# Kernel optimization log

Hardware: AMD Instinct MI355X
Metric: run time of the kernel (lower is better)

Reference implementation:

```python
import jax, jax.numpy as jnp
import numpy as np
import math

DIM = 1024
NUM_HEADS = 16
HEAD_DIM = DIM // NUM_HEADS
ROPE_BASE = 10000.0
LN_EPS = 1e-5


def _rope_tables(seq_len):
    inv_freq = 1.0 / (ROPE_BASE ** (jnp.arange(0, HEAD_DIM, 2, dtype=jnp.float32) / HEAD_DIM))
    t = jnp.arange(seq_len, dtype=jnp.float32)
    freqs = t[:, None] * inv_freq[None, :]            # (T, D/2)
    emb = jnp.concatenate([freqs, freqs], axis=-1)    # (T, D)
    return jnp.cos(emb), jnp.sin(emb)


def _rotate_half(x):
    x1 = x[..., ::2]
    x2 = x[..., 1::2]
    return jnp.stack((-x2, x1), axis=-1).reshape(x.shape)


def _heads(y):
    B, T, _ = y.shape
    return y.reshape(B, T, NUM_HEADS, HEAD_DIM).transpose(0, 2, 1, 3)  # (B,H,T,hd)


def _layernorm(x, w, b):
    mu = jnp.mean(x, axis=-1, keepdims=True)
    var = jnp.var(x, axis=-1, keepdims=True)
    return (x - mu) / jnp.sqrt(var + LN_EPS) * w + b


def setup_inputs() -> dict:
    key = jax.random.key(0)
    ks = jax.random.split(key, 16)
    s = 1.0 / math.sqrt(DIM)
    d = {
        "x": jax.random.normal(ks[0], (2, 2048, DIM), jnp.float32),
        "h_a": jax.random.normal(ks[1], (2, 512, DIM), jnp.float32),
        "h_t": jax.random.normal(ks[2], (2, 64, DIM), jnp.float32),
        "p": jax.random.normal(ks[3], (2, 256, DIM), jnp.float32),
    }
    names = ["Wq", "Wks", "Wvs", "Wka", "Wva", "Wkt", "Wvt", "Wo", "Wf"]
    for i, n in enumerate(names):
        d[n] = jax.random.normal(ks[4 + i], (DIM, DIM), jnp.float32) * s
        d["b" + n[1:]] = jnp.zeros((DIM,), jnp.float32)
    d["gating"] = jnp.zeros((1,), jnp.float32)
    d["ln_w"] = jnp.ones((DIM,), jnp.float32)
    d["ln_b"] = jnp.zeros((DIM,), jnp.float32)
    return d


def reference(x, h_a, h_t, p,
              Wq, bq, Wks, bks, Wvs, bvs, Wka, bka, Wva, bva,
              Wkt, bkt, Wvt, bvt, Wo, bo, Wf, bf,
              gating, ln_w, ln_b):
    B, T, D = x.shape
    g = jnp.tanh(gating)[0]
    h_adapter = jnp.concatenate((h_a, p), axis=1)          # (B, Ta+Tp, D)
    cos, sin = _rope_tables(T)                             # (T, hd)

    q = _heads(x @ Wq + bq)
    ks_ = _heads(x @ Wks + bks)
    vs = _heads(x @ Wvs + bvs)
    q = q * cos + _rotate_half(q) * sin
    ks_ = ks_ * cos + _rotate_half(ks_) * sin

    ka = _heads(h_adapter @ Wka + bka)
    va = _heads(h_adapter @ Wva + bva)
    kt = _heads(h_t @ Wkt + bkt)
    vt = _heads(h_t @ Wvt + bvt)

    s_self = jnp.einsum("bhqd,bhkd->bhqk", q, ks_)
    s_adpt = jnp.einsum("bhqd,bhkd->bhqk", q, ka)
    s_task = jnp.einsum("bhqd,bhkd->bhqk", q, kt) * g
    scores = jnp.concatenate([s_self, s_adpt, s_task], axis=-1) / math.sqrt(HEAD_DIM)
    attn = jax.nn.softmax(scores, axis=-1)                 # (B,H,T,S_total)

    v_all = jnp.concatenate([vs, va, vt], axis=2)          # (B,H,S_total,hd)
    out = jnp.einsum("bhqk,bhkd->bhqd", attn, v_all)
    out = out.transpose(0, 2, 1, 3).reshape(B, T, D)
    out = out @ Wo + bo

    res = _layernorm(out + x, ln_w, ln_b)
    res = jax.nn.relu(res @ Wf + bf)
    return res
```

## Files before the change

kernel.cpp:

```cpp
#include <hip/hip_runtime.h>

typedef __attribute__((ext_vector_type(8))) short bf16x8;
typedef __attribute__((ext_vector_type(4))) float f32x4;
typedef __attribute__((ext_vector_type(8))) unsigned short u16x8;

#define DEV static __device__ __forceinline__

DEV float bf2f(unsigned short u) {
    union { unsigned int i; float f; } x; x.i = ((unsigned int)u) << 16; return x.f;
}
DEV unsigned short f2bf(float f) {
    union { float f; unsigned int i; } x; x.f = f;
    unsigned int r = x.i + 0x7FFFu + ((x.i >> 16) & 1u);
    return (unsigned short)(r >> 16);
}
DEV unsigned int cvt_pk_bf16(float a, float b) {
    unsigned int r;
    asm("v_cvt_pk_bf16_f32 %0, %1, %2" : "=v"(r) : "v"(a), "v"(b));
    return r;
}
DEV float ldany(const void* p, size_t i, bool f32) {
    return f32 ? ((const float*)p)[i] : bf2f(((const unsigned short*)p)[i]);
}

struct Quad { const void* w0; const void* w1; const void* w2; const void* w3; };
struct Tri  { const void* b0; const void* b1; const void* b2; void* o0; void* o1; void* o2; };
struct ExtArgs {
    const void* ha; const void* pp; const void* ht;
    const void* bka; const void* bva; const void* bkt; const void* bvt;
    void* kx; void* vx;
};

__global__ __launch_bounds__(64)
void detect_f32(const unsigned int* __restrict__ w, int* __restrict__ flag)
{
    if (threadIdx.x == 0 && blockIdx.x == 0)
        flag[0] = (w[0] == 0x3F800000u) ? 1 : 0;
}

__global__ __launch_bounds__(256)
void rope_tab(float2* __restrict__ tab)
{
    const int idx = blockIdx.x * 256 + threadIdx.x;
    const int m = idx >> 5, d = idx & 31;
    const float a = (float)m * exp2f(-(float)d * 0.41524101186092033f);
    float sn, cs;
    sincosf(a, &sn, &cs);
    tab[idx] = make_float2(cs, sn);
}

__global__ __launch_bounds__(256)
void transpose_w(Quad q, unsigned short* __restrict__ dstbase, const int* __restrict__ flagp)
{
    const bool dsf = (*flagp != 0);
    const int z = blockIdx.z;
    const void* W = (z == 0) ? q.w0 : (z == 1) ? q.w1 : (z == 2) ? q.w2 : q.w3;
    unsigned short* out = dstbase + ((size_t)z << 20);
    __shared__ unsigned short Ts[64][72];
    const int t = threadIdx.x;
    const int n0 = blockIdx.x * 64, k0 = blockIdx.y * 64;
    const int r = t >> 2, c = (t & 3) << 4;
    if (!dsf) {
        const unsigned short* Wp = (const unsigned short*)W + (size_t)(k0 + r) * 1024 + n0 + c;
        *(u16x8*)&Ts[r][c]     = *(const u16x8*)Wp;
        *(u16x8*)&Ts[r][c + 8] = *(const u16x8*)(Wp + 8);
    } else {
        const float4* Wf4 = (const float4*)((const float*)W + (size_t)(k0 + r) * 1024 + n0 + c);
        float4 f[4];
        #pragma unroll
        for (int j = 0; j < 4; ++j) f[j] = Wf4[j];
        unsigned int* Td = (unsigned int*)&Ts[r][c];
        #pragma unroll
        for (int j = 0; j < 4; ++j) {
            Td[2 * j]     = cvt_pk_bf16(f[j].x, f[j].y);
            Td[2 * j + 1] = cvt_pk_bf16(f[j].z, f[j].w);
        }
    }
    __syncthreads();
    unsigned short tmp[16];
    #pragma unroll
    for (int j = 0; j < 16; ++j) tmp[j] = Ts[c + j][r];
    unsigned short* op = out + (size_t)(n0 + r) * 1024 + k0 + c;
    *(u16x8*)op       = *(const u16x8*)&tmp[0];
    *(u16x8*)(op + 8) = *(const u16x8*)&tmp[8];
}

template<int AMODE, int OMODE, bool RELU, bool ROPEF>
__global__ __launch_bounds__(256)
void gemm_mfma(const void* __restrict__ A, const unsigned short* __restrict__ WTbase,
               Tri t3, const int* __restrict__ flagp, const float2* __restrict__ rtab,
               int mblocks, int rpb_in, int rpb_out, int row_off)
{
    const int K = 1024, N = 1024;
    const bool dsf = (*flagp != 0);
    const bool af32 = (AMODE == 1) && dsf;
    __shared__ unsigned short As[64 * 64];
    __shared__ unsigned short Bs[128 * 64];
    const int tid = threadIdx.x;
    const int z = blockIdx.y / mblocks;
    const int m0 = (blockIdx.y - z * mblocks) * 64;
    const int n0 = blockIdx.x * 128;
    const unsigned short* WT = WTbase + ((size_t)z << 20);
    const void* bias = (z == 0) ? t3.b0 : (z == 1) ? t3.b1 : t3.b2;
    void* Cv = (z == 0) ? t3.o0 : (z == 1) ? t3.o1 : t3.o2;

    const int ar = tid >> 2, aq = (tid & 3) << 1, ah = ar & 7;
    const int br = tid >> 1, bq = (tid & 1) << 2, bh = br & 7;
    const unsigned short* Bg = WT + (size_t)(n0 + br) * K + (bq << 3);
    const size_t arow = (size_t)(m0 + ar) * K + (aq << 3);

    const int lane = tid & 63, wv = tid >> 6;
    const int wm = (wv >> 1) << 5, wn = (wv & 1) << 6;
    const int il = lane & 15, quad = lane >> 4;
    const int h = il & 7;
    const int c0 = ((quad ^ h) << 3);
    int aoff[2], boff[4];
    #pragma unroll
    for (int mi = 0; mi < 2; ++mi) aoff[mi] = (wm + mi * 16 + il) * 64;
    #pragma unroll
    for (int nj = 0; nj < 4; ++nj) boff[nj] = (wn + nj * 16 + il) * 64;

    f32x4 acc[2][4];
    #pragma unroll
    for (int mi = 0; mi < 2; ++mi)
        #pragma unroll
        for (int nj = 0; nj < 4; ++nj) acc[mi][nj] = (f32x4){0.f, 0.f, 0.f, 0.f};

    u16x8 av[2], bv[4];
    auto load_ab = [&](int kq) {
        if (!af32) {
            const unsigned short* Ag = (const unsigned short*)A + arow + kq;
            av[0] = *(const u16x8*)Ag;
            av[1] = *(const u16x8*)(Ag + 8);
        } else {
            const float4* Af4 = (const float4*)((const float*)A + arow + kq);
            float4 f[4];
            #pragma unroll
            for (int j = 0; j < 4; ++j) f[j] = Af4[j];
            #pragma unroll
            for (int j = 0; j < 2; ++j) {
                unsigned int* d = (unsigned int*)&av[j];
                d[0] = cvt_pk_bf16(f[2 * j].x, f[2 * j].y);
                d[1] = cvt_pk_bf16(f[2 * j].z, f[2 * j].w);
                d[2] = cvt_pk_bf16(f[2 * j + 1].x, f[2 * j + 1].y);
                d[3] = cvt_pk_bf16(f[2 * j + 1].z, f[2 * j + 1].w);
            }
        }
        #pragma unroll
        for (int j = 0; j < 4; ++j) bv[j] = *(const u16x8*)(Bg + kq + 8 * j);
    };
    load_ab(0);

    for (int k0 = 0; k0 < K; k0 += 64) {
        __syncthreads();
        *(u16x8*)&As[ar * 64 + ((aq ^ ah) << 3)]       = av[0];
        *(u16x8*)&As[ar * 64 + (((aq ^ 1) ^ ah) << 3)] = av[1];
        #pragma unroll
        for (int j = 0; j < 4; ++j)
            *(u16x8*)&Bs[br * 64 + (((bq ^ j) ^ bh) << 3)] = bv[j];
        __syncthreads();
        load_ab((k0 + 64 < K) ? k0 + 64 : k0);
        #pragma unroll
        for (int kk = 0; kk < 2; ++kk) {
            const int cc = c0 ^ (kk << 5);
            bf16x8 af[2], bfr[4];
            #pragma unroll
            for (int mi = 0; mi < 2; ++mi) af[mi] = *(const bf16x8*)&As[aoff[mi] + cc];
            #pragma unroll
            for (int nj = 0; nj < 4; ++nj) bfr[nj] = *(const bf16x8*)&Bs[boff[nj] + cc];
            #pragma unroll
            for (int mi = 0; mi < 2; ++mi)
                #pragma unroll
                for (int nj = 0; nj < 4; ++nj)
                    acc[mi][nj] = __builtin_amdgcn_mfma_f32_16x16x32_bf16(
                        af[mi], bfr[nj], acc[mi][nj], 0, 0, 0);
        }
    }

    const bool doRope = ROPEF && (z < 2);
    float bval[4];
    #pragma unroll
    for (int nj = 0; nj < 4; ++nj) bval[nj] = ldany(bias, n0 + wn + nj * 16 + il, dsf);
    #pragma unroll
    for (int mi = 0; mi < 2; ++mi) {
        #pragma unroll
        for (int r = 0; r < 4; ++r) {
            const int m = m0 + wm + mi * 16 + quad * 4 + r;
            const int bidx = m / rpb_in;
            const size_t orow = (size_t)bidx * rpb_out + row_off + (m - bidx * rpb_in);
            #pragma unroll
            for (int nj = 0; nj < 4; ++nj) {
                float v = acc[mi][nj][r] + bval[nj];
                if (doRope) {
                    const int dcol = n0 + wn + nj * 16 + il;
                    const float2 cs2 = rtab[((m & 2047) << 5) | (dcol & 31)];
                    const float partner = __shfl_xor(v, 1);
                    v = (il & 1) ? fmaf(v, cs2.x, partner * cs2.y)
                                 : fmaf(v, cs2.x, -partner * cs2.y);
                }
                if (RELU) v = fmaxf(v, 0.0f);
                const size_t idx = orow * N + n0 + wn + nj * 16 + il;
                if (OMODE == 0) ((unsigned short*)Cv)[idx] = f2bf(v);
                else {
                    if (dsf) ((float*)Cv)[idx] = v;
                    else     ((unsigned short*)Cv)[idx] = f2bf(v);
                }
            }
        }
    }
}

__global__ __launch_bounds__(256)
void gemm_ext(ExtArgs ea, const unsigned short* __restrict__ WTbase,
              const int* __restrict__ flagp)
{
    const int K = 1024, N = 1024;
    const bool dsf = (*flagp != 0);
    __shared__ unsigned short As[64 * 64];
    __shared__ unsigned short Bs[128 * 64];
    const int tid = threadIdx.x;
    const int y = blockIdx.y;
    const int w = (y >= 26) ? 1 : 0;
    const int yy = y - w * 26;
    int s, m0b;
    if (yy < 16)      { s = 0; m0b = yy; }
    else if (yy < 24) { s = 1; m0b = yy - 16; }
    else              { s = 2; m0b = yy - 24; }
    const void* A = (s == 0) ? ea.ha : (s == 1) ? ea.pp : ea.ht;
    const int rpb_in  = (s == 0) ? 512 : (s == 1) ? 256 : 64;
    const int row_off = (s == 0) ? 0 : (s == 1) ? 512 : 768;
    const int wtslot = ((s == 2) ? 2 : 0) + w;
    const void* bias = (w == 0) ? ((s == 2) ? ea.bkt : ea.bka)
                                : ((s == 2) ? ea.bvt : ea.bva);
    void* Cv = (w == 0) ? ea.kx : ea.vx;
    const int m0 = m0b * 64;
    const int n0 = blockIdx.x * 128;
    const unsigned short* WT = WTbase + ((size_t)wtslot << 20);

    const int ar = tid >> 2, aq = (tid & 3) << 1, ah = ar & 7;
    const int br = tid >> 1, bq = (tid & 1) << 2, bh = br & 7;
    const unsigned short* Bg = WT + (size_t)(n0 + br) * K + (bq << 3);
    const size_t arow = (size_t)(m0 + ar) * K + (aq << 3);

    const int lane = tid & 63, wv = tid >> 6;
    const int wm = (wv >> 1) << 5, wn = (wv & 1) << 6;
    const int il = lane & 15, quad = lane >> 4;
    const int h = il & 7;
    const int c0 = ((quad ^ h) << 3);
    int aoff[2], boff[4];
    #pragma unroll
    for (int mi = 0; mi < 2; ++mi) aoff[mi] = (wm + mi * 16 + il) * 64;
    #pragma unroll
    for (int nj = 0; nj < 4; ++nj) boff[nj] = (wn + nj * 16 + il) * 64;

    f32x4 acc[2][4];
    #pragma unroll
    for (int mi = 0; mi < 2; ++mi)
        #pragma unroll
        for (int nj = 0; nj < 4; ++nj) acc[mi][nj] = (f32x4){0.f, 0.f, 0.f, 0.f};

    u16x8 av[2], bv[4];
    auto load_ab = [&](int kq) {
        if (!dsf) {
            const unsigned short* Ag = (const unsigned short*)A + arow + kq;
            av[0] = *(const u16x8*)Ag;
            av[1] = *(const u16x8*)(Ag + 8);
        } else {
            const float4* Af4 = (const float4*)((const float*)A + arow + kq);
            float4 f[4];
            #pragma unroll
            for (int j = 0; j < 4; ++j) f[j] = Af4[j];
            #pragma unroll
            for (int j = 0; j < 2; ++j) {
                unsigned int* d = (unsigned int*)&av[j];
                d[0] = cvt_pk_bf16(f[2 * j].x, f[2 * j].y);
                d[1] = cvt_pk_bf16(f[2 * j].z, f[2 * j].w);
                d[2] = cvt_pk_bf16(f[2 * j + 1].x, f[2 * j + 1].y);
                d[3] = cvt_pk_bf16(f[2 * j + 1].z, f[2 * j + 1].w);
            }
        }
        #pragma unroll
        for (int j = 0; j < 4; ++j) bv[j] = *(const u16x8*)(Bg + kq + 8 * j);
    };
    load_ab(0);

    for (int k0 = 0; k0 < K; k0 += 64) {
        __syncthreads();
        *(u16x8*)&As[ar * 64 + ((aq ^ ah) << 3)]       = av[0];
        *(u16x8*)&As[ar * 64 + (((aq ^ 1) ^ ah) << 3)] = av[1];
        #pragma unroll
        for (int j = 0; j < 4; ++j)
            *(u16x8*)&Bs[br * 64 + (((bq ^ j) ^ bh) << 3)] = bv[j];
        __syncthreads();
        load_ab((k0 + 64 < K) ? k0 + 64 : k0);
        #pragma unroll
        for (int kk = 0; kk < 2; ++kk) {
            const int cc = c0 ^ (kk << 5);
            bf16x8 af[2], bfr[4];
            #pragma unroll
            for (int mi = 0; mi < 2; ++mi) af[mi] = *(const bf16x8*)&As[aoff[mi] + cc];
            #pragma unroll
            for (int nj = 0; nj < 4; ++nj) bfr[nj] = *(const bf16x8*)&Bs[boff[nj] + cc];
            #pragma unroll
            for (int mi = 0; mi < 2; ++mi)
                #pragma unroll
                for (int nj = 0; nj < 4; ++nj)
                    acc[mi][nj] = __builtin_amdgcn_mfma_f32_16x16x32_bf16(
                        af[mi], bfr[nj], acc[mi][nj], 0, 0, 0);
        }
    }

    float bval[4];
    #pragma unroll
    for (int nj = 0; nj < 4; ++nj) bval[nj] = ldany(bias, n0 + wn + nj * 16 + il, dsf);
    #pragma unroll
    for (int mi = 0; mi < 2; ++mi) {
        #pragma unroll
        for (int r = 0; r < 4; ++r) {
            const int m = m0 + wm + mi * 16 + quad * 4 + r;
            const int bidx = m / rpb_in;
            const size_t orow = (size_t)bidx * 832 + row_off + (m - bidx * rpb_in);
            #pragma unroll
            for (int nj = 0; nj < 4; ++nj) {
                const float v = acc[mi][nj][r] + bval[nj];
                ((unsigned short*)Cv)[orow * N + n0 + wn + nj * 16 + il] = f2bf(v);
            }
        }
    }
}

__global__ __launch_bounds__(256)
void attn_mfma(const unsigned short* __restrict__ Q, const unsigned short* __restrict__ Ksf,
               const unsigned short* __restrict__ Vsf, const unsigned short* __restrict__ Kx,
               const unsigned short* __restrict__ Vx, const void* __restrict__ gate,
               const int* __restrict__ flagp, unsigned short* __restrict__ AO)
{
    const int T = 2048, TX = 832, D = 1024;
    __shared__ unsigned short Klds[2][64 * 72];
    __shared__ unsigned short Vlds[2][64 * 72];
    __shared__ unsigned short Plds[4][32 * 72];
    const int tid = threadIdx.x;
    const int bh = blockIdx.x;
    const int b = bh >> 4, h = bh & 15;
    const int t0 = blockIdx.y << 7;
    const bool dsf = (*flagp != 0);
    const float g = tanhf(ldany(gate, 0, dsf));

    const int lane = tid & 63, wv = tid >> 6;
    const int il = lane & 15, quad = lane >> 4;
    const int qw = t0 + (wv << 5);

    bf16x8 qf[2][2];
    #pragma unroll
    for (int mi = 0; mi < 2; ++mi) {
        const unsigned short* qp =
            Q + (size_t)(b * T + qw + mi * 16 + il) * D + (h << 6) + quad * 8;
        qf[mi][0] = *(const bf16x8*)qp;
        qf[mi][1] = *(const bf16x8*)(qp + 32);
    }
    bf16x8 ones;
    #pragma unroll
    for (int e = 0; e < 8; ++e) ((unsigned short*)&ones)[e] = 0x3F80;

    const int ksr = tid >> 2, ksd = (tid & 3) << 4;
    const int vkey = tid & 63, vdb = (tid >> 6) << 4;
    const int vpos = (vkey & 15) * 4 + (vkey >> 4);

    f32x4 o[2][4], ol[2];
    #pragma unroll
    for (int mi = 0; mi < 2; ++mi) {
        ol[mi] = (f32x4){0.f, 0.f, 0.f, 0.f};
        #pragma unroll
        for (int dt = 0; dt < 4; ++dt) o[mi][dt] = (f32x4){0.f, 0.f, 0.f, 0.f};
    }

    u16x8 kr0, kr1, vr0, vr1;
    auto load_kv = [&](int kt) {
        const unsigned short *kp, *vp;
        if (kt < 32) {
            kp = Ksf + (size_t)(b * T + (kt << 6) + ksr) * D + (h << 6) + ksd;
            vp = Vsf + (size_t)(b * T + (kt << 6) + vkey) * D + (h << 6) + vdb;
        } else {
            kp = Kx + (size_t)(b * TX + ((kt - 32) << 6) + ksr) * D + (h << 6) + ksd;
            vp = Vx + (size_t)(b * TX + ((kt - 32) << 6) + vkey) * D + (h << 6) + vdb;
        }
        kr0 = *(const u16x8*)kp; kr1 = *(const u16x8*)(kp + 8);
        vr0 = *(const u16x8*)vp; vr1 = *(const u16x8*)(vp + 8);
    };
    load_kv(0);

    #pragma unroll 1
    for (int kt = 0; kt < 45; ++kt) {
        const int cur = kt & 1;
        *(u16x8*)&Klds[cur][ksr * 72 + ksd]     = kr0;
        *(u16x8*)&Klds[cur][ksr * 72 + ksd + 8] = kr1;
        #pragma unroll
        for (int j = 0; j < 8; ++j)
            Vlds[cur][(vdb + j) * 72 + vpos]     = ((unsigned short*)&vr0)[j];
        #pragma unroll
        for (int j = 0; j < 8; ++j)
            Vlds[cur][(vdb + 8 + j) * 72 + vpos] = ((unsigned short*)&vr1)[j];
        __syncthreads();
        if (kt < 44) load_kv(kt + 1);

        f32x4 s[2][4];
        #pragma unroll
        for (int mi = 0; mi < 2; ++mi)
            #pragma unroll
            for (int ct = 0; ct < 4; ++ct) s[mi][ct] = (f32x4){0.f, 0.f, 0.f, 0.f};
        #pragma unroll
        for (int ct = 0; ct < 4; ++ct) {
            #pragma unroll
            for (int c = 0; c < 2; ++c) {
                bf16x8 kf = *(const bf16x8*)&Klds[cur][(ct * 16 + il) * 72 + c * 32 + quad * 8];
                #pragma unroll
                for (int mi = 0; mi < 2; ++mi)
                    s[mi][ct] = __builtin_amdgcn_mfma_f32_16x16x32_bf16(
                        qf[mi][c], kf, s[mi][ct], 0, 0, 0);
            }
        }
        const float fc = ((kt == 44) ? g : 1.0f) * 0.18033688011112042f;

        #pragma unroll
        for (int mi = 0; mi < 2; ++mi)
            #pragma unroll
            for (int r = 0; r < 4; ++r) {
                const float e0 = exp2f(fmaf(s[mi][0][r], fc, -11.541560327111708f));
                const float e1 = exp2f(fmaf(s[mi][1][r], fc, -11.541560327111708f));
                const float e2 = exp2f(fmaf(s[mi][2][r], fc, -11.541560327111708f));
                const float e3 = exp2f(fmaf(s[mi][3][r], fc, -11.541560327111708f));
                const unsigned int lo = cvt_pk_bf16(e0, e1);
                const unsigned int hi = cvt_pk_bf16(e2, e3);
                *(uint2*)&Plds[wv][(mi * 16 + quad * 4 + r) * 72 + (il << 2)] =
                    make_uint2(lo, hi);
            }

        #pragma unroll
        for (int c = 0; c < 2; ++c) {
            bf16x8 pf[2];
            #pragma unroll
            for (int mi = 0; mi < 2; ++mi)
                pf[mi] = *(const bf16x8*)&Plds[wv][(mi * 16 + il) * 72 + c * 32 + quad * 8];
            #pragma unroll
            for (int mi = 0; mi < 2; ++mi)
                ol[mi] = __builtin_amdgcn_mfma_f32_16x16x32_bf16(pf[mi], ones, ol[mi], 0, 0, 0);
            #pragma unroll
            for (int dt = 0; dt < 4; ++dt) {
                bf16x8 vf = *(const bf16x8*)&Vlds[cur][(dt * 16 + il) * 72 + c * 32 + quad * 8];
                #pragma unroll
                for (int mi = 0; mi < 2; ++mi)
                    o[mi][dt] = __builtin_amdgcn_mfma_f32_16x16x32_bf16(
                        pf[mi], vf, o[mi][dt], 0, 0, 0);
            }
        }
    }

    #pragma unroll
    for (int mi = 0; mi < 2; ++mi) {
        float invl[4];
        #pragma unroll
        for (int r = 0; r < 4; ++r) invl[r] = 1.0f / ol[mi][r];
        #pragma unroll
        for (int dt = 0; dt < 4; ++dt)
            #pragma unroll
            for (int r = 0; r < 4; ++r)
                AO[(size_t)(b * T + qw + mi * 16 + quad * 4 + r) * D + (h << 6) + dt * 16 + il] =
                    f2bf(o[mi][dt][r] * invl[r]);
    }
}

__global__ __launch_bounds__(256)
void ln_res(const unsigned short* __restrict__ proj, const void* __restrict__ x,
            const void* __restrict__ w, const void* __restrict__ bb,
            const int* __restrict__ flagp, unsigned short* __restrict__ y)
{
    const int row = blockIdx.x;
    const int tid = threadIdx.x;
    const bool dsf = (*flagp != 0);
    const unsigned short* pr = proj + (size_t)row * 1024;
    float v[4];
    #pragma unroll
    for (int e = 0; e < 4; ++e)
        v[e] = bf2f(pr[(tid << 2) + e]) + ldany(x, (size_t)row * 1024 + (tid << 2) + e, dsf);
    float s1 = v[0] + v[1] + v[2] + v[3];
    float s2 = v[0]*v[0] + v[1]*v[1] + v[2]*v[2] + v[3]*v[3];
    #pragma unroll
    for (int off = 1; off < 64; off <<= 1) {
        s1 += __shfl_xor(s1, off);
        s2 += __shfl_xor(s2, off);
    }
    __shared__ float red1[4], red2[4];
    const int wv = tid >> 6;
    if ((tid & 63) == 0) { red1[wv] = s1; red2[wv] = s2; }
    __syncthreads();
    s1 = red1[0] + red1[1] + red1[2] + red1[3];
    s2 = red2[0] + red2[1] + red2[2] + red2[3];
    const float mu = s1 * (1.0f / 1024.0f);
    const float var = s2 * (1.0f / 1024.0f) - mu * mu;
    const float rstd = rsqrtf(var + 1e-5f);
    #pragma unroll
    for (int e = 0; e < 4; ++e) {
        const int d = (tid << 2) + e;
        const float yy = (v[e] - mu) * rstd * ldany(w, d, dsf) + ldany(bb, d, dsf);
        y[(size_t)row * 1024 + d] = f2bf(yy);
    }
}

extern "C" void kernel_launch(void* const* d_in, const int* in_sizes, int n_in,
                              void* d_out, int out_size, void* d_ws, size_t ws_size,
                              hipStream_t stream)
{
    const void* x    = d_in[0];
    const void* h_a  = d_in[1];
    const void* h_t  = d_in[2];
    const void* p    = d_in[3];
    const void* Wq   = d_in[4];
    const void* bq   = d_in[5];
    const void* Wks  = d_in[6];
    const void* bks  = d_in[7];
    const void* Wvs  = d_in[8];
    const void* bvs  = d_in[9];
    const void* Wka  = d_in[10];
    const void* bka  = d_in[11];
    const void* Wva  = d_in[12];
    const void* bva  = d_in[13];
    const void* Wkt  = d_in[14];
    const void* bkt  = d_in[15];
    const void* Wvt  = d_in[16];
    const void* bvt  = d_in[17];
    const void* Wo   = d_in[18];
    const void* bo   = d_in[19];
    const void* Wf   = d_in[20];
    const void* bf_  = d_in[21];
    const void* gating = d_in[22];
    const void* ln_w = d_in[23];
    const void* ln_b = d_in[24];

    char* ws = (char*)d_ws;
    int*            flag = (int*)ws;
    unsigned short* qb   = (unsigned short*)(ws + 256);
    unsigned short* ks   = (unsigned short*)(ws + 8388864);
    unsigned short* vs   = (unsigned short*)(ws + 16777472);
    unsigned short* kx   = (unsigned short*)(ws + 25166080);
    unsigned short* vx   = (unsigned short*)(ws + 28573952);
    unsigned short* ao   = (unsigned short*)(ws + 31981824);
    unsigned short* proj  = ks;
    unsigned short* lnout = vs;
    unsigned short* WT1 = ao;
    unsigned short* WT3 = kx;
    float2*         rtab = (float2*)kx;

    dim3 blk(256);
    const Tri nul = {};

    detect_f32<<<1, 64, 0, stream>>>((const unsigned int*)ln_w, flag);

    rope_tab<<<256, blk, 0, stream>>>(rtab);

    transpose_w<<<dim3(16, 16, 3), blk, 0, stream>>>(Quad{Wq, Wks, Wvs, Wvs}, WT1, flag);
    {
        Tri t3 = {bq, bks, bvs, qb, ks, vs};
        gemm_mfma<1, 0, false, true><<<dim3(8, 64 * 3), blk, 0, stream>>>(
            x, WT1, t3, flag, rtab, 64, 4096, 4096, 0);
    }

    transpose_w<<<dim3(16, 16, 4), blk, 0, stream>>>(Quad{Wka, Wva, Wkt, Wvt}, WT1, flag);
    {
        ExtArgs ea = {h_a, p, h_t, bka, bva, bkt, bvt, kx, vx};
        gemm_ext<<<dim3(8, 52), blk, 0, stream>>>(ea, WT1, flag);
    }

    attn_mfma<<<dim3(32, 16), blk, 0, stream>>>(qb, ks, vs, kx, vx, gating, flag, ao);

    transpose_w<<<dim3(16, 16, 2), blk, 0, stream>>>(Quad{Wo, Wf, Wf, Wf}, WT3, flag);
    {
        Tri t3 = {bo, nul.b1, nul.b2, proj, nul.o1, nul.o2};
        gemm_mfma<0, 0, false, false><<<dim3(8, 64), blk, 0, stream>>>(
            ao, WT3, t3, flag, nullptr, 64, 4096, 4096, 0);
    }
    ln_res<<<4096, blk, 0, stream>>>(proj, x, ln_w, ln_b, flag, lnout);
    {
        Tri t3 = {bf_, nul.b1, nul.b2, d_out, nul.o1, nul.o2};
        gemm_mfma<0, 2, true, false><<<dim3(8, 64), blk, 0, stream>>>(
            lnout, WT3 + ((size_t)1 << 20), t3, flag, nullptr, 64, 4096, 4096, 0);
    }
}
```

Baseline: 389.7 us.

## Double-buffer GEMM LDS with direct global-to-LDS loads, vectorize LN, merge detect kernel

Both GEMM kernels now use double-buffered LDS tiles. The weight (B) tile is staged with global_load_lds direct-to-LDS copies, using an XOR swizzle applied on the source address, so the next tile loads while the current one is consumed and one barrier per k-step is dropped. The A tile is also loaded direct to LDS when it is bf16; the fp32 path keeps register conversion one step ahead. LayerNorm loads and stores are vectorized, and the dtype-detect kernel is folded into rope_tab to save a launch. Shared memory doubles, which may reduce occupancy, and the swizzle must match the existing read pattern.

New measurement: 373.3 us. -4.2%, faster.

```diff
diff --git a/kernel.cpp b/kernel.cpp
--- a/kernel.cpp
+++ b/kernel.cpp
@@ -3,6 +3,7 @@
 typedef __attribute__((ext_vector_type(8))) short bf16x8;
 typedef __attribute__((ext_vector_type(4))) float f32x4;
 typedef __attribute__((ext_vector_type(8))) unsigned short u16x8;
+typedef __attribute__((ext_vector_type(4))) unsigned short u16x4;
 
 #define DEV static __device__ __forceinline__
 
@@ -21,6 +22,13 @@
 }
 DEV float ldany(const void* p, size_t i, bool f32) {
     return f32 ? ((const float*)p)[i] : bf2f(((const unsigned short*)p)[i]);
+}
+DEV void gload16(const void* g, void* l) {
+    __builtin_amdgcn_global_load_lds(
+        (const __attribute__((address_space(1))) unsigned int*)g,
+        reinterpret_cast<__attribute__((address_space(3))) unsigned int*>(
+            reinterpret_cast<uintptr_t>(l)),
+        16, 0, 0);
 }
 
 struct Quad { const void* w0; const void* w1; const void* w2; const void* w3; };
@@ -31,17 +39,12 @@
     void* kx; void* vx;
 };
 
-__global__ __launch_bounds__(64)
-void detect_f32(const unsigned int* __restrict__ w, int* __restrict__ flag)
-{
-    if (threadIdx.x == 0 && blockIdx.x == 0)
-        flag[0] = (w[0] == 0x3F800000u) ? 1 : 0;
-}
-
 __global__ __launch_bounds__(256)
-void rope_tab(float2* __restrict__ tab)
+void rope_tab(float2* __restrict__ tab, const unsigned int* __restrict__ wchk,
+              int* __restrict__ flag)
 {
     const int idx = blockIdx.x * 256 + threadIdx.x;
+    if (idx == 0) flag[0] = (wchk[0] == 0x3F800000u) ? 1 : 0;
     const int m = idx >> 5, d = idx & 31;
     const float a = (float)m * exp2f(-(float)d * 0.41524101186092033f);
     float sn, cs;
@@ -94,8 +97,8 @@
     const int K = 1024, N = 1024;
     const bool dsf = (*flagp != 0);
     const bool af32 = (AMODE == 1) && dsf;
-    __shared__ unsigned short As[64 * 64];
-    __shared__ unsigned short Bs[128 * 64];
+    __shared__ unsigned short As[2][64 * 64];
+    __shared__ unsigned short Bs[2][128 * 64];
     const int tid = threadIdx.x;
     const int z = blockIdx.y / mblocks;
     const int m0 = (blockIdx.y - z * mblocks) * 64;
@@ -104,12 +107,22 @@
     const void* bias = (z == 0) ? t3.b0 : (z == 1) ? t3.b1 : t3.b2;
     void* Cv = (z == 0) ? t3.o0 : (z == 1) ? t3.o1 : t3.o2;
 
+    const int lane = tid & 63, wv = tid >> 6;
+    const int l3 = lane >> 3, c8 = lane & 7;
+    const int swz = (c8 ^ l3) << 3;
+
+    const unsigned short* Bsrc[4];
+    #pragma unroll
+    for (int j = 0; j < 4; ++j)
+        Bsrc[j] = WT + (size_t)(n0 + (wv << 5) + (j << 3) + l3) * K + swz;
+    const unsigned short* Asrc[2];
+    #pragma unroll
+    for (int j = 0; j < 2; ++j)
+        Asrc[j] = (const unsigned short*)A + (size_t)(m0 + (wv << 4) + (j << 3) + l3) * K + swz;
+
     const int ar = tid >> 2, aq = (tid & 3) << 1, ah = ar & 7;
-    const int br = tid >> 1, bq = (tid & 1) << 2, bh = br & 7;
-    const unsigned short* Bg = WT + (size_t)(n0 + br) * K + (bq << 3);
     const size_t arow = (size_t)(m0 + ar) * K + (aq << 3);
 
-    const int lane = tid & 63, wv = tid >> 6;
     const int wm = (wv >> 1) << 5, wn = (wv & 1) << 6;
     const int il = lane & 15, quad = lane >> 4;
     const int h = il & 7;
@@ -126,8 +139,8 @@
         #pragma unroll
         for (int nj = 0; nj < 4; ++nj) acc[mi][nj] = (f32x4){0.f, 0.f, 0.f, 0.f};
 
-    u16x8 av[2], bv[4];
-    auto load_ab = [&](int kq) {
+    u16x8 av[2];
+    auto loadA = [&](int kq) {
         if (!af32) {
             const unsigned short* Ag = (const unsigned short*)A + arow + kq;
             av[0] = *(const u16x8*)Ag;
@@ -146,28 +159,43 @@
                 d[3] = cvt_pk_bf16(f[2 * j + 1].z, f[2 * j + 1].w);
             }
         }
-        #pragma unroll
-        for (int j = 0; j < 4; ++j) bv[j] = *(const u16x8*)(Bg + kq + 8 * j);
-    };
-    load_ab(0);
+    };
+    auto writeA = [&](int buf) {
+        *(u16x8*)&As[buf][ar * 64 + ((aq ^ ah) << 3)]       = av[0];
+        *(u16x8*)&As[buf][ar * 64 + (((aq ^ 1) ^ ah) << 3)] = av[1];
+    };
+    auto stageB = [&](int buf, int k0) {
+        #pragma unroll
+        for (int j = 0; j < 4; ++j)
+            gload16(Bsrc[j] + k0, &Bs[buf][((wv << 2) + j) << 9]);
+    };
+    auto stageA = [&](int buf, int k0) {
+        #pragma unroll
+        for (int j = 0; j < 2; ++j)
+            gload16(Asrc[j] + k0, &As[buf][((wv << 1) + j) << 9]);
+    };
+
+    if (AMODE == 1) loadA(0);
+    stageB(0, 0);
+    if (AMODE == 1) { writeA(0); loadA(64); }
+    else            stageA(0, 0);
+    __syncthreads();
 
     for (int k0 = 0; k0 < K; k0 += 64) {
-        __syncthreads();
-        *(u16x8*)&As[ar * 64 + ((aq ^ ah) << 3)]       = av[0];
-        *(u16x8*)&As[ar * 64 + (((aq ^ 1) ^ ah) << 3)] = av[1];
-        #pragma unroll
-        for (int j = 0; j < 4; ++j)
-            *(u16x8*)&Bs[br * 64 + (((bq ^ j) ^ bh) << 3)] = bv[j];
-        __syncthreads();
-        load_ab((k0 + 64 < K) ? k0 + 64 : k0);
+        const int cur = (k0 >> 6) & 1;
+        if (k0 + 64 < K) {
+            stageB(cur ^ 1, k0 + 64);
+            if (AMODE == 1) { writeA(cur ^ 1); if (k0 + 128 < K) loadA(k0 + 128); }
+            else            stageA(cur ^ 1, k0 + 64);
+        }
         #pragma unroll
         for (int kk = 0; kk < 2; ++kk) {
             const int cc = c0 ^ (kk << 5);
             bf16x8 af[2], bfr[4];
             #pragma unroll
-            for (int mi = 0; mi < 2; ++mi) af[mi] = *(const bf16x8*)&As[aoff[mi] + cc];
-            #pragma unroll
-            for (int nj = 0; nj < 4; ++nj) bfr[nj] = *(const bf16x8*)&Bs[boff[nj] + cc];
+            for (int mi = 0; mi < 2; ++mi) af[mi] = *(const bf16x8*)&As[cur][aoff[mi] + cc];
+            #pragma unroll
+            for (int nj = 0; nj < 4; ++nj) bfr[nj] = *(const bf16x8*)&Bs[cur][boff[nj] + cc];
             #pragma unroll
             for (int mi = 0; mi < 2; ++mi)
                 #pragma unroll
@@ -175,6 +203,7 @@
                     acc[mi][nj] = __builtin_amdgcn_mfma_f32_16x16x32_bf16(
                         af[mi], bfr[nj], acc[mi][nj], 0, 0, 0);
         }
+        __syncthreads();
     }
 
     const bool doRope = ROPEF && (z < 2);
@@ -216,8 +245,8 @@
 {
     const int K = 1024, N = 1024;
     const bool dsf = (*flagp != 0);
-    __shared__ unsigned short As[64 * 64];
-    __shared__ unsigned short Bs[128 * 64];
+    __shared__ unsigned short As[2][64 * 64];
+    __shared__ unsigned short Bs[2][128 * 64];
     const int tid = threadIdx.x;
     const int y = blockIdx.y;
     const int w = (y >= 26) ? 1 : 0;
@@ -237,12 +266,18 @@
     const int n0 = blockIdx.x * 128;
     const unsigned short* WT = WTbase + ((size_t)wtslot << 20);
 
+    const int lane = tid & 63, wv = tid >> 6;
+    const int l3 = lane >> 3, c8 = lane & 7;
+    const int swz = (c8 ^ l3) << 3;
+
+    const unsigned short* Bsrc[4];
+    #pragma unroll
+    for (int j = 0; j < 4; ++j)
+        Bsrc[j] = WT + (size_t)(n0 + (wv << 5) + (j << 3) + l3) * K + swz;
+
     const int ar = tid >> 2, aq = (tid & 3) << 1, ah = ar & 7;
-    const int br = tid >> 1, bq = (tid & 1) << 2, bh = br & 7;
-    const unsigned short* Bg = WT + (size_t)(n0 + br) * K + (bq << 3);
     const size_t arow = (size_t)(m0 + ar) * K + (aq << 3);
 
-    const int lane = tid & 63, wv = tid >> 6;
     const int wm = (wv >> 1) << 5, wn = (wv & 1) << 6;
     const int il = lane & 15, quad = lane >> 4;
     const int h = il & 7;
@@ -259,8 +294,8 @@
         #pragma unroll
         for (int nj = 0; nj < 4; ++nj) acc[mi][nj] = (f32x4){0.f, 0.f, 0.f, 0.f};
 
-    u16x8 av[2], bv[4];
-    auto load_ab = [&](int kq) {
+    u16x8 av[2];
+    auto loadA = [&](int kq) {
         if (!dsf) {
             const unsigned short* Ag = (const unsigned short*)A + arow + kq;
             av[0] = *(const u16x8*)Ag;
@@ -279,28 +314,37 @@
                 d[3] = cvt_pk_bf16(f[2 * j + 1].z, f[2 * j + 1].w);
             }
         }
-        #pragma unroll
-        for (int j = 0; j < 4; ++j) bv[j] = *(const u16x8*)(Bg + kq + 8 * j);
-    };
-    load_ab(0);
+    };
+    auto writeA = [&](int buf) {
+        *(u16x8*)&As[buf][ar * 64 + ((aq ^ ah) << 3)]       = av[0];
+        *(u16x8*)&As[buf][ar * 64 + (((aq ^ 1) ^ ah) << 3)] = av[1];
+    };
+    auto stageB = [&](int buf, int k0) {
+        #pragma unroll
+        for (int j = 0; j < 4; ++j)
+            gload16(Bsrc[j] + k0, &Bs[buf][((wv << 2) + j) << 9]);
+    };
+
+    loadA(0);
+    stageB(0, 0);
+    writeA(0); loadA(64);
+    __syncthreads();
 
     for (int k0 = 0; k0 < K; k0 += 64) {
-        __syncthreads();
-        *(u16x8*)&As[ar * 64 + ((aq ^ ah) << 3)]       = av[0];
-        *(u16x8*)&As[ar * 64 + (((aq ^ 1) ^ ah) << 3)] = av[1];
-        #pragma unroll
-        for (int j = 0; j < 4; ++j)
-            *(u16x8*)&Bs[br * 64 + (((bq ^ j) ^ bh) << 3)] = bv[j];
-        __syncthreads();
-        load_ab((k0 + 64 < K) ? k0 + 64 : k0);
+        const int cur = (k0 >> 6) & 1;
+        if (k0 + 64 < K) {
+            stageB(cur ^ 1, k0 + 64);
+            writeA(cur ^ 1);
+            if (k0 + 128 < K) loadA(k0 + 128);
+        }
         #pragma unroll
         for (int kk = 0; kk < 2; ++kk) {
             const int cc = c0 ^ (kk << 5);
             bf16x8 af[2], bfr[4];
             #pragma unroll
-            for (int mi = 0; mi < 2; ++mi) af[mi] = *(const bf16x8*)&As[aoff[mi] + cc];
-            #pragma unroll
-            for (int nj = 0; nj < 4; ++nj) bfr[nj] = *(const bf16x8*)&Bs[boff[nj] + cc];
+            for (int mi = 0; mi < 2; ++mi) af[mi] = *(const bf16x8*)&As[cur][aoff[mi] + cc];
+            #pragma unroll
+            for (int nj = 0; nj < 4; ++nj) bfr[nj] = *(const bf16x8*)&Bs[cur][boff[nj] + cc];
             #pragma unroll
             for (int mi = 0; mi < 2; ++mi)
                 #pragma unroll
@@ -308,6 +352,7 @@
                     acc[mi][nj] = __builtin_amdgcn_mfma_f32_16x16x32_bf16(
                         af[mi], bfr[nj], acc[mi][nj], 0, 0, 0);
         }
+        __syncthreads();
     }
 
     float bval[4];
@@ -478,10 +523,17 @@
     const int tid = threadIdx.x;
     const bool dsf = (*flagp != 0);
     const unsigned short* pr = proj + (size_t)row * 1024;
+    const u16x4 p4 = *(const u16x4*)(pr + (tid << 2));
     float v[4];
-    #pragma unroll
-    for (int e = 0; e < 4; ++e)
-        v[e] = bf2f(pr[(tid << 2) + e]) + ldany(x, (size_t)row * 1024 + (tid << 2) + e, dsf);
+    if (dsf) {
+        const float4 x4 = *(const float4*)((const float*)x + (size_t)row * 1024 + (tid << 2));
+        v[0] = bf2f(p4[0]) + x4.x; v[1] = bf2f(p4[1]) + x4.y;
+        v[2] = bf2f(p4[2]) + x4.z; v[3] = bf2f(p4[3]) + x4.w;
+    } else {
+        const u16x4 x4 = *(const u16x4*)((const unsigned short*)x + (size_t)row * 1024 + (tid << 2));
+        #pragma unroll
+        for (int e = 0; e < 4; ++e) v[e] = bf2f(p4[e]) + bf2f(x4[e]);
+    }
     float s1 = v[0] + v[1] + v[2] + v[3];
     float s2 = v[0]*v[0] + v[1]*v[1] + v[2]*v[2] + v[3]*v[3];
     #pragma unroll
@@ -498,12 +550,23 @@
     const float mu = s1 * (1.0f / 1024.0f);
     const float var = s2 * (1.0f / 1024.0f) - mu * mu;
     const float rstd = rsqrtf(var + 1e-5f);
-    #pragma unroll
-    for (int e = 0; e < 4; ++e) {
-        const int d = (tid << 2) + e;
-        const float yy = (v[e] - mu) * rstd * ldany(w, d, dsf) + ldany(bb, d, dsf);
-        y[(size_t)row * 1024 + d] = f2bf(yy);
-    }
+    float wv4[4], bv4[4];
+    if (dsf) {
+        const float4 wf = *(const float4*)((const float*)w + (tid << 2));
+        const float4 bf4 = *(const float4*)((const float*)bb + (tid << 2));
+        wv4[0] = wf.x; wv4[1] = wf.y; wv4[2] = wf.z; wv4[3] = wf.w;
+        bv4[0] = bf4.x; bv4[1] = bf4.y; bv4[2] = bf4.z; bv4[3] = bf4.w;
+    } else {
+        const u16x4 wf = *(const u16x4*)((const unsigned short*)w + (tid << 2));
+        const u16x4 bf4 = *(const u16x4*)((const unsigned short*)bb + (tid << 2));
+        #pragma unroll
+        for (int e = 0; e < 4; ++e) { wv4[e] = bf2f(wf[e]); bv4[e] = bf2f(bf4[e]); }
+    }
+    u16x4 o4;
+    #pragma unroll
+    for (int e = 0; e < 4; ++e)
+        o4[e] = f2bf((v[e] - mu) * rstd * wv4[e] + bv4[e]);
+    *(u16x4*)(y + (size_t)row * 1024 + (tid << 2)) = o4;
 }
 
 extern "C" void kernel_launch(void* const* d_in, const int* in_sizes, int n_in,
@@ -553,9 +616,7 @@
     dim3 blk(256);
     const Tri nul = {};
 
-    detect_f32<<<1, 64, 0, stream>>>((const unsigned int*)ln_w, flag);
-
-    rope_tab<<<256, blk, 0, stream>>>(rtab);
+    rope_tab<<<256, blk, 0, stream>>>(rtab, (const unsigned int*)ln_w, flag);
 
     transpose_w<<<dim3(16, 16, 3), blk, 0, stream>>>(Quad{Wq, Wks, Wvs, Wvs}, WT1, flag);
     {
```
